# Kernel tuning notes

Measured on AMD Instinct MI355X. Metric: run time of the kernel, lower is better.

Reference implementation:

```python
import jax, jax.numpy as jnp
import numpy as np
import math

H, DK, DV = 16, 64, 64
D = H * DK  # model_dimension = 1024
N = M = L = 2048


def setup_inputs() -> dict:
    key = jax.random.key(0)
    ks = jax.random.split(key, 12)
    s = 1.0 / math.sqrt(DK)  # keep softmax logits in a sane range
    return {
        "queries": jax.random.normal(ks[0], (N, DK), jnp.float32),
        "keys": jax.random.normal(ks[1], (M, DK), jnp.float32),
        "values": jax.random.normal(ks[2], (L, DV), jnp.float32),
        "Wq": jax.random.normal(ks[3], (H, DK, D), jnp.float32) * s,
        "bq": jax.random.normal(ks[4], (H, D), jnp.float32) * 0.02,
        "Wk": jax.random.normal(ks[5], (H, DK, D), jnp.float32) * s,
        "bk": jax.random.normal(ks[6], (H, D), jnp.float32) * 0.02,
        "Wv": jax.random.normal(ks[7], (H, DV, D), jnp.float32) * s,
        "bv": jax.random.normal(ks[8], (H, D), jnp.float32) * 0.02,
        "Wo": jax.random.normal(ks[9], (D, H * DV), jnp.float32) * (1.0 / math.sqrt(H * DV)),
        "bo": jax.random.normal(ks[10], (D,), jnp.float32) * 0.02,
    }


def reference(queries, keys, values, Wq, bq, Wk, bk, Wv, bv, Wo, bo):
    # Batched per-head projections (original loops over heads in Python).
    Qp = jnp.einsum("nk,hkd->hnd", queries, Wq) + bq[:, None, :]   # (H, N, D)
    Kp = jnp.einsum("mk,hkd->hmd", keys, Wk) + bk[:, None, :]      # (H, M, D)
    Vp = jnp.einsum("lv,hvd->hld", values, Wv) + bv[:, None, :]    # (H, M, D)
    scores = jnp.einsum("hnd,hmd->hnm", Qp, Kp) / math.sqrt(DK)
    attn = jax.nn.softmax(scores, axis=-1)
    heads_out = jnp.einsum("hnm,hmd->hnd", attn, Vp)               # (H, N, D)
    # torch.concat(heads, dim=0).sum(dim=0) == sum over heads AND rows -> (D,)
    pooled = heads_out.sum(axis=(0, 1)).reshape(1, D)
    return pooled @ Wo.T + bo  # (1, D)
```

## Files before the change

### kernel.cpp

```cpp
#include <hip/hip_runtime.h>


typedef __attribute__((ext_vector_type(4))) float floatx4;
typedef __attribute__((ext_vector_type(8))) short shortx8;

__device__ inline unsigned short f2bf(float f) {
    unsigned int u = __float_as_uint(f);
    u += 0x7FFFu + ((u >> 16) & 1u);
    return (unsigned short)(u >> 16);
}
__device__ inline float bf2f(unsigned short s) {
    return __uint_as_float(((unsigned int)s) << 16);
}

__global__ __launch_bounds__(256) void prep_kernel(
    const float* __restrict__ Wq, const float* __restrict__ Wk,
    const float* __restrict__ bq, const float* __restrict__ keys,
    const float* __restrict__ values,
    float* __restrict__ Apart, float* __restrict__ vhpart,
    unsigned short* __restrict__ Kb, unsigned short* __restrict__ VT,
    float* __restrict__ r_ws) {
    const int tid = threadIdx.x;
    const int bx = blockIdx.x;
    __shared__ __align__(16) unsigned char sm[36352];
    if (bx < 128) {
        const int g = bx >> 4, h = bx & 15;
        const int c0 = g * 128;
        unsigned short* wq = (unsigned short*)sm;
        unsigned short* wk = (unsigned short*)(sm + 17408);
        float* bqs = (float*)(sm + 34816);
        float* vred = (float*)(sm + 35328);
        {
            int row = tid >> 2, cs = (tid & 3) * 32;
            const float* wqp = Wq + (size_t)(h * 64 + row) * 1024 + c0 + cs;
            const float* wkp = Wk + (size_t)(h * 64 + row) * 1024 + c0 + cs;
            #pragma unroll
            for (int u = 0; u < 8; ++u) {
                float4 a = *(const float4*)&wqp[u * 4];
                float4 b = *(const float4*)&wkp[u * 4];
                *(ushort4*)&wq[row * 136 + cs + u * 4] =
                    (ushort4){f2bf(a.x), f2bf(a.y), f2bf(a.z), f2bf(a.w)};
                *(ushort4*)&wk[row * 136 + cs + u * 4] =
                    (ushort4){f2bf(b.x), f2bf(b.y), f2bf(b.z), f2bf(b.w)};
            }
            if (tid < 128) bqs[tid] = bq[h * 1024 + c0 + tid];
        }
        __syncthreads();
        const int w = tid >> 6, lane = tid & 63;
        const int ln = lane & 15, quad = lane >> 4;
        {
            const int j = tid & 63, half = tid >> 6;
            float accv = 0.f;
            #pragma unroll
            for (int u = 0; u < 32; ++u)
                accv += bf2f(wk[j * 136 + half * 32 + u]) * bqs[half * 32 + u];
            vred[half * 64 + j] = accv;
        }
        shortx8 af[4];
        #pragma unroll
        for (int kk = 0; kk < 4; ++kk)
            af[kk] = *(shortx8*)&wq[(w * 16 + ln) * 136 + kk * 32 + quad * 8];
        float* ap = Apart + (size_t)bx * 4096;
        #pragma unroll
        for (int cn = 0; cn < 4; ++cn) {
            floatx4 acc = {};
            #pragma unroll
            for (int kk = 0; kk < 4; ++kk) {
                shortx8 bf_ = *(shortx8*)&wk[(cn * 16 + ln) * 136 + kk * 32 + quad * 8];
                acc = __builtin_amdgcn_mfma_f32_16x16x32_bf16(af[kk], bf_, acc, 0, 0, 0);
            }
            #pragma unroll
            for (int r = 0; r < 4; ++r)
                ap[(w * 16 + quad * 4 + r) * 64 + cn * 16 + ln] = acc[r];
        }
        __syncthreads();
        if (tid < 64)
            vhpart[bx * 64 + tid] = vred[tid] + vred[64 + tid] +
                                    vred[128 + tid] + vred[192 + tid];
    } else if (bx < 144) {
        int bk = bx - 128;
        int base = (bk * 256 + tid) * 32;
        #pragma unroll
        for (int u = 0; u < 8; ++u) {
            float4 a = *(const float4*)&keys[base + u * 4];
            *(ushort4*)&Kb[base + u * 4] =
                (ushort4){f2bf(a.x), f2bf(a.y), f2bf(a.z), f2bf(a.w)};
        }
        if (tid < 64) r_ws[bk * 64 + tid] = 0.f;
    } else {
        int bb = bx - 144, m0 = bb * 64;
        unsigned short* vts = (unsigned short*)sm;
        #pragma unroll
        for (int it = 0; it < 4; ++it) {
            int gi = tid + it * 256;
            int m = gi >> 4, c4 = (gi & 15) * 4;
            float4 a = *(const float4*)&values[(size_t)(m0 + m) * 64 + c4];
            vts[(c4 + 0) * 72 + m] = f2bf(a.x);
            vts[(c4 + 1) * 72 + m] = f2bf(a.y);
            vts[(c4 + 2) * 72 + m] = f2bf(a.z);
            vts[(c4 + 3) * 72 + m] = f2bf(a.w);
        }
        __syncthreads();
        #pragma unroll
        for (int it = 0; it < 2; ++it) {
            int gi = tid + it * 256;
            int v = gi >> 3, seg = (gi & 7) * 8;
            *(shortx8*)&VT[v * 2048 + m0 + seg] = *(shortx8*)&vts[v * 72 + seg];
        }
    }
}

__global__ __launch_bounds__(256, 2) void flash_kernel(
    const float* __restrict__ queries, const float* __restrict__ Apart,
    const float* __restrict__ vhpart, const unsigned short* __restrict__ Kb,
    const unsigned short* __restrict__ VT, float* __restrict__ r_ws) {
    const int h = blockIdx.y;
    const int n0 = blockIdx.x * 64;
    const int tid = threadIdx.x;
    const int w = tid >> 6, lane = tid & 63;
    const int ln = lane & 15, quad = lane >> 4;
    const int cw = w >> 1;
    const int rw = w & 1;

    __shared__ __align__(16) unsigned char lds[64512];
    __shared__ float vhs[64];
    unsigned short* qh = (unsigned short*)(lds + 36864);
    unsigned short* Pw = (unsigned short*)(lds + 46080 + w * 4608);
    unsigned short* qstage = (unsigned short*)(lds + 46080);
    unsigned short* Atl = (unsigned short*)(lds + 55296);

    {
        int row = tid >> 2, c16 = (tid & 3) * 16;
        const float* qp = queries + (size_t)(n0 + row) * 64 + c16;
        #pragma unroll
        for (int u = 0; u < 4; ++u) {
            float4 a = *(const float4*)&qp[u * 4];
            *(ushort4*)&qstage[row * 72 + c16 + u * 4] =
                (ushort4){f2bf(a.x), f2bf(a.y), f2bf(a.z), f2bf(a.w)};
        }
    }
    {
        int i = tid >> 2, j0 = (tid & 3) * 16;
        const float* ap = Apart + h * 4096 + i * 64 + j0;
        #pragma unroll
        for (int u = 0; u < 16; ++u) {
            float s = 0.f;
            #pragma unroll
            for (int g = 0; g < 8; ++g) s += ap[g * 65536 + u];
            Atl[(j0 + u) * 72 + i] = f2bf(s);
        }
        if (tid < 64) {
            float s = 0.f;
            #pragma unroll
            for (int g = 0; g < 8; ++g) s += vhpart[(g * 16 + h) * 64 + tid];
            vhs[tid] = s;
        }
    }
    const int sb = tid >> 7, si = tid & 127;
    shortx8 sv[4];
    #pragma unroll
    for (int jj = 0; jj < 4; ++jj) {
        int slot = si + jj * 128;
        int v = slot >> 3, seg = (slot & 7) * 8;
        sv[jj] = *(const shortx8*)&VT[v * 2048 + sb * 1024 + seg];
    }
    __syncthreads();

    {
        shortx8 qa[2];
        #pragma unroll
        for (int kk = 0; kk < 2; ++kk)
            qa[kk] = *(shortx8*)&qstage[(w * 16 + ln) * 72 + kk * 32 + quad * 8];
        #pragma unroll
        for (int cn = 0; cn < 4; ++cn) {
            floatx4 acc = {};
            #pragma unroll
            for (int kk = 0; kk < 2; ++kk) {
                shortx8 bfr = *(shortx8*)&Atl[(cn * 16 + ln) * 72 + kk * 32 + quad * 8];
                acc = __builtin_amdgcn_mfma_f32_16x16x32_bf16(qa[kk], bfr, acc, 0, 0, 0);
            }
            #pragma unroll
            for (int r = 0; r < 4; ++r)
                qh[(w * 16 + quad * 4 + r) * 72 + cn * 16 + ln] =
                    f2bf((acc[r] + vhs[cn * 16 + ln]) * 0.125f);
        }
    }
    #pragma unroll
    for (int jj = 0; jj < 4; ++jj) {
        int slot = si + jj * 128;
        int v = slot >> 3, seg = (slot & 7) * 8;
        *(shortx8*)&((unsigned short*)(lds + sb * 9216))[v * 72 + seg] = sv[jj];
        sv[jj] = *(const shortx8*)&VT[v * 2048 + sb * 1024 + 64 + seg];
    }
    __syncthreads();

    shortx8 qf[2][2];
    #pragma unroll
    for (int t = 0; t < 2; ++t)
        #pragma unroll
        for (int kk = 0; kk < 2; ++kk)
            qf[t][kk] = *(shortx8*)&qh[(rw * 32 + t * 16 + ln) * 72 + kk * 32 + quad * 8];
    shortx8 pk[8];
    #pragma unroll
    for (int cm = 0; cm < 4; ++cm)
        #pragma unroll
        for (int kk = 0; kk < 2; ++kk)
            pk[cm * 2 + kk] = *(const shortx8*)
                &Kb[(size_t)(cw * 1024 + cm * 16 + ln) * 64 + kk * 32 + quad * 8];

    floatx4 O0[4] = {}, O1[4] = {};
    float lacc0[4] = {}, lacc1[4] = {};

    for (int s = 0; s < 16; ++s) {
        floatx4 S0[4], S1[4];
        #pragma unroll
        for (int cm = 0; cm < 4; ++cm) {
            floatx4 a0 = {}, a1 = {};
            a0 = __builtin_amdgcn_mfma_f32_16x16x32_bf16(qf[0][0], pk[cm * 2], a0, 0, 0, 0);
            a0 = __builtin_amdgcn_mfma_f32_16x16x32_bf16(qf[0][1], pk[cm * 2 + 1], a0, 0, 0, 0);
            a1 = __builtin_amdgcn_mfma_f32_16x16x32_bf16(qf[1][0], pk[cm * 2], a1, 0, 0, 0);
            a1 = __builtin_amdgcn_mfma_f32_16x16x32_bf16(qf[1][1], pk[cm * 2 + 1], a1, 0, 0, 0);
            S0[cm] = a0; S1[cm] = a1;
        }
        if (s < 15) {
            int m0n = cw * 1024 + (s + 1) * 64;
            #pragma unroll
            for (int cm = 0; cm < 4; ++cm)
                #pragma unroll
                for (int kk = 0; kk < 2; ++kk)
                    pk[cm * 2 + kk] = *(const shortx8*)
                        &Kb[(size_t)(m0n + cm * 16 + ln) * 64 + kk * 32 + quad * 8];
        }
        if (s < 15) {
            unsigned short* vb = (unsigned short*)(lds + (((s + 1) & 1) * 2 + sb) * 9216);
            int s2 = (s + 2 <= 15) ? (s + 2) : 15;
            #pragma unroll
            for (int jj = 0; jj < 4; ++jj) {
                int slot = si + jj * 128;
                int v = slot >> 3, seg = (slot & 7) * 8;
                *(shortx8*)&vb[v * 72 + seg] = sv[jj];
                sv[jj] = *(const shortx8*)&VT[v * 2048 + sb * 1024 + s2 * 64 + seg];
            }
        }
        #pragma unroll
        for (int cm = 0; cm < 4; ++cm) {
            #pragma unroll
            for (int r = 0; r < 4; ++r) {
                float p0 = __expf(S0[cm][r]); lacc0[r] += p0;
                Pw[(quad * 4 + r) * 72 + cm * 16 + ln] = f2bf(p0);
                float p1 = __expf(S1[cm][r]); lacc1[r] += p1;
                Pw[(16 + quad * 4 + r) * 72 + cm * 16 + ln] = f2bf(p1);
            }
        }
        shortx8 pf[2][2];
        #pragma unroll
        for (int t = 0; t < 2; ++t)
            #pragma unroll
            for (int kk = 0; kk < 2; ++kk)
                pf[t][kk] = *(shortx8*)&Pw[(t * 16 + ln) * 72 + kk * 32 + quad * 8];
        const unsigned short* vb = (const unsigned short*)(lds + ((s & 1) * 2 + cw) * 9216);
        #pragma unroll
        for (int cv = 0; cv < 4; ++cv) {
            shortx8 v0 = *(const shortx8*)&vb[(cv * 16 + ln) * 72 + quad * 8];
            shortx8 v1 = *(const shortx8*)&vb[(cv * 16 + ln) * 72 + 32 + quad * 8];
            O0[cv] = __builtin_amdgcn_mfma_f32_16x16x32_bf16(pf[0][0], v0, O0[cv], 0, 0, 0);
            O0[cv] = __builtin_amdgcn_mfma_f32_16x16x32_bf16(pf[0][1], v1, O0[cv], 0, 0, 0);
            O1[cv] = __builtin_amdgcn_mfma_f32_16x16x32_bf16(pf[1][0], v0, O1[cv], 0, 0, 0);
            O1[cv] = __builtin_amdgcn_mfma_f32_16x16x32_bf16(pf[1][1], v1, O1[cv], 0, 0, 0);
        }
        __syncthreads();
    }

    float lr0[4], lr1[4];
    #pragma unroll
    for (int r = 0; r < 4; ++r) {
        float x0 = lacc0[r], x1 = lacc1[r];
        #pragma unroll
        for (int o = 1; o <= 8; o <<= 1) { x0 += __shfl_xor(x0, o); x1 += __shfl_xor(x1, o); }
        lr0[r] = x0; lr1[r] = x1;
    }
    float* Obuf = (float*)lds;
    float* LSUM = (float*)(lds + 36864);
    float* LINV = (float*)(lds + 37376);
    #pragma unroll
    for (int cv = 0; cv < 4; ++cv)
        #pragma unroll
        for (int r = 0; r < 4; ++r) {
            Obuf[(w * 32 + quad * 4 + r) * 68 + cv * 16 + ln] = O0[cv][r];
            Obuf[(w * 32 + 16 + quad * 4 + r) * 68 + cv * 16 + ln] = O1[cv][r];
        }
    if (ln == 0) {
        #pragma unroll
        for (int r = 0; r < 4; ++r) {
            LSUM[w * 32 + quad * 4 + r] = lr0[r];
            LSUM[w * 32 + 16 + quad * 4 + r] = lr1[r];
        }
    }
    __syncthreads();
    if (tid < 64) LINV[tid] = 1.0f / (LSUM[tid] + LSUM[64 + tid]);
    __syncthreads();
    {
        int v = tid & 63, grp = tid >> 6;
        float acc = 0.f;
        #pragma unroll
        for (int u = 0; u < 16; ++u) {
            int g = grp * 16 + u;
            acc += (Obuf[g * 68 + v] + Obuf[(64 + g) * 68 + v]) * LINV[g];
        }
        atomicAdd(&r_ws[h * 64 + v], acc);
    }
}

__global__ __launch_bounds__(256) void pool_kernel(
    const float* __restrict__ Wv, const float* __restrict__ bv,
    const float* __restrict__ r_ws, float* __restrict__ pooled) {
    const int tid = threadIdx.x;
    const int d0 = blockIdx.x * 16;
    const int d = tid & 15, hh = tid >> 4;
    __shared__ float red[16][17];
    float acc = bv[hh * 1024 + d0 + d] * 2048.0f;
    const float* rv = r_ws + hh * 64;
    const float* wp = Wv + (size_t)hh * 64 * 1024 + d0 + d;
    #pragma unroll 8
    for (int v = 0; v < 64; ++v) acc += rv[v] * wp[(size_t)v * 1024];
    red[hh][d] = acc;
    __syncthreads();
    if (tid < 16) {
        float s = 0.f;
        #pragma unroll
        for (int g = 0; g < 16; ++g) s += red[g][tid];
        pooled[d0 + tid] = s;
    }
}

__global__ __launch_bounds__(256) void out_kernel(
    const float* __restrict__ Wo, const float* __restrict__ bo,
    const float* __restrict__ pooled, float* __restrict__ out) {
    const int tid = threadIdx.x, w = tid >> 6, lane = tid & 63;
    const int dp = blockIdx.x * 4 + w;
    const float* wr = Wo + (size_t)dp * 1024 + lane * 16;
    const float* pp = pooled + lane * 16;
    float acc = 0.f;
    #pragma unroll
    for (int u = 0; u < 4; ++u) {
        float4 a = *(const float4*)&wr[u * 4];
        float4 p = *(const float4*)&pp[u * 4];
        acc += a.x * p.x + a.y * p.y + a.z * p.z + a.w * p.w;
    }
    #pragma unroll
    for (int o = 32; o > 0; o >>= 1) acc += __shfl_xor(acc, o);
    if (lane == 0) out[dp] = acc + bo[dp];
}

extern "C" void kernel_launch(void* const* d_in, const int* in_sizes, int n_in,
                              void* d_out, int out_size, void* d_ws, size_t ws_size,
                              hipStream_t stream) {
    const float* queries = (const float*)d_in[0];
    const float* keys    = (const float*)d_in[1];
    const float* values  = (const float*)d_in[2];
    const float* Wq      = (const float*)d_in[3];
    const float* bq      = (const float*)d_in[4];
    const float* Wk      = (const float*)d_in[5];
    const float* Wv      = (const float*)d_in[7];
    const float* bv      = (const float*)d_in[8];
    const float* Wo      = (const float*)d_in[9];
    const float* bo      = (const float*)d_in[10];
    float* out = (float*)d_out;

    float* Apart  = (float*)d_ws;
    float* vhpart = Apart + 524288;
    float* r_ws   = vhpart + 8192;
    float* pooled = r_ws + 1024;
    unsigned short* Kb = (unsigned short*)(pooled + 1024);
    unsigned short* VT = Kb + 131072;

    prep_kernel<<<176, 256, 0, stream>>>(Wq, Wk, bq, keys, values,
                                         Apart, vhpart, Kb, VT, r_ws);
    flash_kernel<<<dim3(32, 16), 256, 0, stream>>>(queries, Apart, vhpart,
                                                   Kb, VT, r_ws);
    pool_kernel<<<64, 256, 0, stream>>>(Wv, bv, r_ws, pooled);
    out_kernel<<<256, 256, 0, stream>>>(Wo, bo, pooled, out);
}
```

Measured before the change: 141.7 us.

## Split flash kernel into 32-row tiles with 4-way key split and register V loads

The flash kernel now handles 32 query rows per block instead of 64, which doubles the grid. Each of the four waves covers a quarter of the keys (512) across 8 steps rather than sharing rows across two key halves. V tiles are read from global memory straight into registers, replacing the LDS double-buffered staging and its per-step __syncthreads. Softmax now uses exp2 with log2(e) folded into the Q scale, the P buffer stride is padded, and LDS use is cut so three blocks can fit per CU. The trade-off is more redundant per-block setup (the A tile reduction is repeated per block) and uncoalesced global V loads.

```diff
diff --git a/kernel.cpp b/kernel.cpp
--- a/kernel.cpp
+++ b/kernel.cpp
@@ -110,34 +110,37 @@
     }
 }
 
-__global__ __launch_bounds__(256, 2) void flash_kernel(
+#define QSCALE 0.18033688f
+__global__ __launch_bounds__(256, 3) void flash_kernel(
     const float* __restrict__ queries, const float* __restrict__ Apart,
     const float* __restrict__ vhpart, const unsigned short* __restrict__ Kb,
     const unsigned short* __restrict__ VT, float* __restrict__ r_ws) {
     const int h = blockIdx.y;
-    const int n0 = blockIdx.x * 64;
+    const int n0 = blockIdx.x * 32;
     const int tid = threadIdx.x;
     const int w = tid >> 6, lane = tid & 63;
     const int ln = lane & 15, quad = lane >> 4;
-    const int cw = w >> 1;
-    const int rw = w & 1;
-
-    __shared__ __align__(16) unsigned char lds[64512];
+    const int cw = w;
+
+    __shared__ __align__(16) unsigned char lds[35456];
     __shared__ float vhs[64];
-    unsigned short* qh = (unsigned short*)(lds + 36864);
-    unsigned short* Pw = (unsigned short*)(lds + 46080 + w * 4608);
-    unsigned short* qstage = (unsigned short*)(lds + 46080);
-    unsigned short* Atl = (unsigned short*)(lds + 55296);
+    unsigned short* qstage = (unsigned short*)lds;
+    unsigned short* Atl = (unsigned short*)(lds + 4608);
+    unsigned short* qh  = (unsigned short*)(lds + 19456);
+    unsigned short* Pw  = (unsigned short*)(lds + w * 4864);
+    float* Obuf = (float*)lds;
+    float* LSUM = (float*)(lds + 34816);
+    float* LINV = (float*)(lds + 35328);
 
     {
-        int row = tid >> 2, c16 = (tid & 3) * 16;
-        const float* qp = queries + (size_t)(n0 + row) * 64 + c16;
-        #pragma unroll
-        for (int u = 0; u < 4; ++u) {
-            float4 a = *(const float4*)&qp[u * 4];
-            *(ushort4*)&qstage[row * 72 + c16 + u * 4] =
-                (ushort4){f2bf(a.x), f2bf(a.y), f2bf(a.z), f2bf(a.w)};
-        }
+        int row = tid >> 3, c8 = (tid & 7) * 8;
+        const float* qp = queries + (size_t)(n0 + row) * 64 + c8;
+        float4 a = *(const float4*)qp;
+        float4 b = *(const float4*)(qp + 4);
+        *(ushort4*)&qstage[row * 72 + c8] =
+            (ushort4){f2bf(a.x), f2bf(a.y), f2bf(a.z), f2bf(a.w)};
+        *(ushort4*)&qstage[row * 72 + c8 + 4] =
+            (ushort4){f2bf(b.x), f2bf(b.y), f2bf(b.z), f2bf(b.w)};
     }
     {
         int i = tid >> 2, j0 = (tid & 3) * 16;
@@ -156,23 +159,17 @@
             vhs[tid] = s;
         }
     }
-    const int sb = tid >> 7, si = tid & 127;
-    shortx8 sv[4];
-    #pragma unroll
-    for (int jj = 0; jj < 4; ++jj) {
-        int slot = si + jj * 128;
-        int v = slot >> 3, seg = (slot & 7) * 8;
-        sv[jj] = *(const shortx8*)&VT[v * 2048 + sb * 1024 + seg];
-    }
     __syncthreads();
 
     {
+        const int t = w & 1, cnb = (w >> 1) * 2;
         shortx8 qa[2];
         #pragma unroll
         for (int kk = 0; kk < 2; ++kk)
-            qa[kk] = *(shortx8*)&qstage[(w * 16 + ln) * 72 + kk * 32 + quad * 8];
-        #pragma unroll
-        for (int cn = 0; cn < 4; ++cn) {
+            qa[kk] = *(shortx8*)&qstage[(t * 16 + ln) * 72 + kk * 32 + quad * 8];
+        #pragma unroll
+        for (int i = 0; i < 2; ++i) {
+            int cn = cnb + i;
             floatx4 acc = {};
             #pragma unroll
             for (int kk = 0; kk < 2; ++kk) {
@@ -181,16 +178,9 @@
             }
             #pragma unroll
             for (int r = 0; r < 4; ++r)
-                qh[(w * 16 + quad * 4 + r) * 72 + cn * 16 + ln] =
-                    f2bf((acc[r] + vhs[cn * 16 + ln]) * 0.125f);
-        }
-    }
-    #pragma unroll
-    for (int jj = 0; jj < 4; ++jj) {
-        int slot = si + jj * 128;
-        int v = slot >> 3, seg = (slot & 7) * 8;
-        *(shortx8*)&((unsigned short*)(lds + sb * 9216))[v * 72 + seg] = sv[jj];
-        sv[jj] = *(const shortx8*)&VT[v * 2048 + sb * 1024 + 64 + seg];
+                qh[(t * 16 + quad * 4 + r) * 72 + cn * 16 + ln] =
+                    f2bf((acc[r] + vhs[cn * 16 + ln]) * QSCALE);
+        }
     }
     __syncthreads();
 
@@ -199,19 +189,22 @@
     for (int t = 0; t < 2; ++t)
         #pragma unroll
         for (int kk = 0; kk < 2; ++kk)
-            qf[t][kk] = *(shortx8*)&qh[(rw * 32 + t * 16 + ln) * 72 + kk * 32 + quad * 8];
-    shortx8 pk[8];
+            qf[t][kk] = *(shortx8*)&qh[(t * 16 + ln) * 72 + kk * 32 + quad * 8];
+
+    const unsigned short* KbC = Kb + (size_t)(cw * 512) * 64;
+    const unsigned short* VTC = VT + cw * 512;
+    shortx8 pk[8], pv[8];
     #pragma unroll
     for (int cm = 0; cm < 4; ++cm)
         #pragma unroll
         for (int kk = 0; kk < 2; ++kk)
             pk[cm * 2 + kk] = *(const shortx8*)
-                &Kb[(size_t)(cw * 1024 + cm * 16 + ln) * 64 + kk * 32 + quad * 8];
+                &KbC[(size_t)(cm * 16 + ln) * 64 + kk * 32 + quad * 8];
 
     floatx4 O0[4] = {}, O1[4] = {};
     float lacc0[4] = {}, lacc1[4] = {};
 
-    for (int s = 0; s < 16; ++s) {
+    for (int s = 0; s < 8; ++s) {
         floatx4 S0[4], S1[4];
         #pragma unroll
         for (int cm = 0; cm < 4; ++cm) {
@@ -222,53 +215,47 @@
             a1 = __builtin_amdgcn_mfma_f32_16x16x32_bf16(qf[1][1], pk[cm * 2 + 1], a1, 0, 0, 0);
             S0[cm] = a0; S1[cm] = a1;
         }
-        if (s < 15) {
-            int m0n = cw * 1024 + (s + 1) * 64;
+        {
+            int mb = s * 64;
+            #pragma unroll
+            for (int cv = 0; cv < 4; ++cv)
+                #pragma unroll
+                for (int hf = 0; hf < 2; ++hf)
+                    pv[cv * 2 + hf] = *(const shortx8*)
+                        &VTC[(size_t)(cv * 16 + ln) * 2048 + mb + hf * 32 + quad * 8];
+        }
+        if (s < 7) {
+            int mb = (s + 1) * 64;
             #pragma unroll
             for (int cm = 0; cm < 4; ++cm)
                 #pragma unroll
                 for (int kk = 0; kk < 2; ++kk)
                     pk[cm * 2 + kk] = *(const shortx8*)
-                        &Kb[(size_t)(m0n + cm * 16 + ln) * 64 + kk * 32 + quad * 8];
-        }
-        if (s < 15) {
-            unsigned short* vb = (unsigned short*)(lds + (((s + 1) & 1) * 2 + sb) * 9216);
-            int s2 = (s + 2 <= 15) ? (s + 2) : 15;
-            #pragma unroll
-            for (int jj = 0; jj < 4; ++jj) {
-                int slot = si + jj * 128;
-                int v = slot >> 3, seg = (slot & 7) * 8;
-                *(shortx8*)&vb[v * 72 + seg] = sv[jj];
-                sv[jj] = *(const shortx8*)&VT[v * 2048 + sb * 1024 + s2 * 64 + seg];
+                        &KbC[(size_t)(mb + cm * 16 + ln) * 64 + kk * 32 + quad * 8];
+        }
+        #pragma unroll
+        for (int cm = 0; cm < 4; ++cm) {
+            #pragma unroll
+            for (int r = 0; r < 4; ++r) {
+                float p0 = __builtin_amdgcn_exp2f(S0[cm][r]); lacc0[r] += p0;
+                Pw[(quad * 4 + r) * 76 + cm * 16 + ln] = f2bf(p0);
+                float p1 = __builtin_amdgcn_exp2f(S1[cm][r]); lacc1[r] += p1;
+                Pw[(16 + quad * 4 + r) * 76 + cm * 16 + ln] = f2bf(p1);
             }
         }
-        #pragma unroll
-        for (int cm = 0; cm < 4; ++cm) {
-            #pragma unroll
-            for (int r = 0; r < 4; ++r) {
-                float p0 = __expf(S0[cm][r]); lacc0[r] += p0;
-                Pw[(quad * 4 + r) * 72 + cm * 16 + ln] = f2bf(p0);
-                float p1 = __expf(S1[cm][r]); lacc1[r] += p1;
-                Pw[(16 + quad * 4 + r) * 72 + cm * 16 + ln] = f2bf(p1);
-            }
-        }
         shortx8 pf[2][2];
         #pragma unroll
         for (int t = 0; t < 2; ++t)
             #pragma unroll
             for (int kk = 0; kk < 2; ++kk)
-                pf[t][kk] = *(shortx8*)&Pw[(t * 16 + ln) * 72 + kk * 32 + quad * 8];
-        const unsigned short* vb = (const unsigned short*)(lds + ((s & 1) * 2 + cw) * 9216);
+                pf[t][kk] = *(shortx8*)&Pw[(t * 16 + ln) * 76 + kk * 32 + quad * 8];
         #pragma unroll
         for (int cv = 0; cv < 4; ++cv) {
-            shortx8 v0 = *(const shortx8*)&vb[(cv * 16 + ln) * 72 + quad * 8];
-            shortx8 v1 = *(const shortx8*)&vb[(cv * 16 + ln) * 72 + 32 + quad * 8];
-            O0[cv] = __builtin_amdgcn_mfma_f32_16x16x32_bf16(pf[0][0], v0, O0[cv], 0, 0, 0);
-            O0[cv] = __builtin_amdgcn_mfma_f32_16x16x32_bf16(pf[0][1], v1, O0[cv], 0, 0, 0);
-            O1[cv] = __builtin_amdgcn_mfma_f32_16x16x32_bf16(pf[1][0], v0, O1[cv], 0, 0, 0);
-            O1[cv] = __builtin_amdgcn_mfma_f32_16x16x32_bf16(pf[1][1], v1, O1[cv], 0, 0, 0);
-        }
-        __syncthreads();
+            O0[cv] = __builtin_amdgcn_mfma_f32_16x16x32_bf16(pf[0][0], pv[cv * 2], O0[cv], 0, 0, 0);
+            O0[cv] = __builtin_amdgcn_mfma_f32_16x16x32_bf16(pf[0][1], pv[cv * 2 + 1], O0[cv], 0, 0, 0);
+            O1[cv] = __builtin_amdgcn_mfma_f32_16x16x32_bf16(pf[1][0], pv[cv * 2], O1[cv], 0, 0, 0);
+            O1[cv] = __builtin_amdgcn_mfma_f32_16x16x32_bf16(pf[1][1], pv[cv * 2 + 1], O1[cv], 0, 0, 0);
+        }
     }
 
     float lr0[4], lr1[4];
@@ -279,33 +266,34 @@
         for (int o = 1; o <= 8; o <<= 1) { x0 += __shfl_xor(x0, o); x1 += __shfl_xor(x1, o); }
         lr0[r] = x0; lr1[r] = x1;
     }
-    float* Obuf = (float*)lds;
-    float* LSUM = (float*)(lds + 36864);
-    float* LINV = (float*)(lds + 37376);
+    __syncthreads();
     #pragma unroll
     for (int cv = 0; cv < 4; ++cv)
         #pragma unroll
         for (int r = 0; r < 4; ++r) {
-            Obuf[(w * 32 + quad * 4 + r) * 68 + cv * 16 + ln] = O0[cv][r];
-            Obuf[(w * 32 + 16 + quad * 4 + r) * 68 + cv * 16 + ln] = O1[cv][r];
+            Obuf[(cw * 32 + quad * 4 + r) * 68 + cv * 16 + ln] = O0[cv][r];
+            Obuf[(cw * 32 + 16 + quad * 4 + r) * 68 + cv * 16 + ln] = O1[cv][r];
         }
     if (ln == 0) {
         #pragma unroll
         for (int r = 0; r < 4; ++r) {
-            LSUM[w * 32 + quad * 4 + r] = lr0[r];
-            LSUM[w * 32 + 16 + quad * 4 + r] = lr1[r];
-        }
-    }
-    __syncthreads();
-    if (tid < 64) LINV[tid] = 1.0f / (LSUM[tid] + LSUM[64 + tid]);
+            LSUM[cw * 32 + quad * 4 + r] = lr0[r];
+            LSUM[cw * 32 + 16 + quad * 4 + r] = lr1[r];
+        }
+    }
+    __syncthreads();
+    if (tid < 32)
+        LINV[tid] = 1.0f / (LSUM[tid] + LSUM[32 + tid] + LSUM[64 + tid] + LSUM[96 + tid]);
     __syncthreads();
     {
         int v = tid & 63, grp = tid >> 6;
         float acc = 0.f;
         #pragma unroll
-        for (int u = 0; u < 16; ++u) {
-            int g = grp * 16 + u;
-            acc += (Obuf[g * 68 + v] + Obuf[(64 + g) * 68 + v]) * LINV[g];
+        for (int u = 0; u < 8; ++u) {
+            int row = grp * 8 + u;
+            float o = Obuf[row * 68 + v] + Obuf[(32 + row) * 68 + v] +
+                      Obuf[(64 + row) * 68 + v] + Obuf[(96 + row) * 68 + v];
+            acc += o * LINV[row];
         }
         atomicAdd(&r_ws[h * 64 + v], acc);
     }
@@ -376,7 +364,7 @@
 
     prep_kernel<<<176, 256, 0, stream>>>(Wq, Wk, bq, keys, values,
                                          Apart, vhpart, Kb, VT, r_ws);
-    flash_kernel<<<dim3(32, 16), 256, 0, stream>>>(queries, Apart, vhpart,
+    flash_kernel<<<dim3(64, 16), 256, 0, stream>>>(queries, Apart, vhpart,
                                                    Kb, VT, r_ws);
     pool_kernel<<<64, 256, 0, stream>>>(Wv, bv, r_ws, pooled);
     out_kernel<<<256, 256, 0, stream>>>(Wo, bo, pooled, out);
```

Result: slower. 172.0 us (+21.4%).
